# Optimization experiments

Measured on AMD Instinct MI355X. Metric: run time of the kernel, lower is better.

## Reference

```python
import jax, jax.numpy as jnp
import numpy as np

B, HIST, PRED = 16, 336, 48
S = HIST + PRED                      # 384 = max_seq_length
H, NL, NH, FF = 768, 12, 12, 3072    # default BertConfig
SA_NH = 16                           # attention_heads arg for the extra SelfAttention
V = 40000                            # num_location_ids
NE = 8                               # num_experts
D_DAY, D_TIME, D_DOW, D_WD, D_LOC = 64, 64, 64, 32, 256
D_IN = D_DAY + D_TIME + D_DOW + D_WD + D_LOC + 1  # 481


def _ln(x, g, b, eps):
    m = jnp.mean(x, -1, keepdims=True)
    v = jnp.mean(jnp.square(x - m), -1, keepdims=True)
    return (x - m) * jax.lax.rsqrt(v + eps) * g + b


def _mha(x, qW, qb, kW, kb, vW, vb, nh):
    b_, s_, h_ = x.shape
    hd = h_ // nh
    q = (x @ qW + qb).reshape(b_, s_, nh, hd)
    k = (x @ kW + kb).reshape(b_, s_, nh, hd)
    v = (x @ vW + vb).reshape(b_, s_, nh, hd)
    scores = jnp.einsum('bqhd,bkhd->bhqk', q, k) / jnp.sqrt(jnp.float32(hd))
    probs = jax.nn.softmax(scores, axis=-1)
    return jnp.einsum('bhqk,bkhd->bqhd', probs, v).reshape(b_, s_, h_)


FLOAT_NAMES = ['day_emb', 'time_emb', 'dow_emb', 'wd_emb', 'loc_emb',
               'ln_in_g', 'ln_in_b', 'inp_W', 'inp_b', 'res_W', 'res_b',
               'sa_qW', 'sa_qb', 'sa_kW', 'sa_kb', 'sa_vW', 'sa_vb', 'sa_oW', 'sa_ob', 'sa_lng', 'sa_lnb',
               'pos_emb', 'tt_emb', 'be_lng', 'be_lnb',
               'bqW', 'bqb', 'bkW', 'bkb', 'bvW', 'bvb', 'boW', 'bob', 'balng', 'balnb',
               'bf1W', 'bf1b', 'bf2W', 'bf2b', 'bflng', 'bflnb',
               'moe_W', 'moe_b', 'gate_W', 'gate_b', 'out_W', 'out_b']


def _forward(floats, ints):
    (day_emb, time_emb, dow_emb, wd_emb, loc_emb,
     ln_in_g, ln_in_b, inp_W, inp_b, res_W, res_b,
     sa_qW, sa_qb, sa_kW, sa_kb, sa_vW, sa_vb, sa_oW, sa_ob, sa_lng, sa_lnb,
     pos_emb, tt_emb, be_lng, be_lnb,
     bqW, bqb, bkW, bkb, bvW, bvb, boW, bob, balng, balnb,
     bf1W, bf1b, bf2W, bf2b, bflng, bflnb,
     moe_W, moe_b, gate_W, gate_b, out_W, out_b) = floats
    isf, hloc, psf = ints

    def feat(f):
        return (day_emb[f[:, :, 0]], time_emb[f[:, :, 1]], dow_emb[f[:, :, 3]],
                wd_emb[f[:, :, 4]], f[:, :, 5].astype(jnp.float32)[..., None])
    hd_, ht_, hw_, hwd_, hdl = feat(isf)
    hist = jnp.concatenate([hd_, ht_, hw_, hwd_, hdl, loc_emb[hloc]], -1)
    fd_, ft_, fw_, fwd_, fdl = feat(psf)
    fut_loc = jnp.zeros((psf.shape[0], psf.shape[1], D_LOC), jnp.float32)  # unknown future locations
    fut = jnp.concatenate([fd_, ft_, fw_, fwd_, fdl, fut_loc], -1)
    x = jnp.concatenate([hist, fut], 1)            # [B,S,481]
    x = _ln(x, ln_in_g, ln_in_b, 1e-5)             # layer_norm on raw features (dropout = identity in eval)
    proj = x @ inp_W + inp_b                       # input_projection -> [B,S,768]
    res = x @ res_W + res_b                        # residual_fc -> [B,S,768]

    # extra SelfAttention block (16 heads) with post-LN residual
    ctx = _mha(proj, sa_qW, sa_qb, sa_kW, sa_kb, sa_vW, sa_vb, SA_NH)
    h = _ln(ctx @ sa_oW + sa_ob + proj, sa_lng, sa_lnb, 1e-5)

    # BERT encoder (inputs_embeds path): add position + token_type(0) embeddings, then 12 post-LN layers
    h = _ln(h + pos_emb[None] + tt_emb, be_lng, be_lnb, 1e-12)
    for i in range(NL):
        ctx = _mha(h, bqW[i], bqb[i], bkW[i], bkb[i], bvW[i], bvb[i], NH)
        a = _ln(ctx @ boW[i] + bob[i] + h, balng[i], balnb[i], 1e-12)
        ff = jax.nn.gelu(a @ bf1W[i] + bf1b[i], approximate=False) @ bf2W[i] + bf2b[i]
        h = _ln(ff + a, bflng[i], bflnb[i], 1e-12)

    # dense soft-MoE: every expert runs on every token, softmax-gated sum
    xf = h.reshape(-1, H)                                                 # [B*S, H]
    eo = jax.nn.gelu(jnp.einsum('nd,edh->neh', xf, moe_W) + moe_b[None], approximate=False)
    gp = jax.nn.softmax(xf @ gate_W + gate_b, axis=-1)                     # [B*S, E]
    moe_out = jnp.einsum('ne,neh->nh', gp, eo).reshape(h.shape)

    logits = (moe_out + res) @ out_W + out_b                               # [B,S,V]
    return logits[:, HIST:, :]                                             # predictions for future slots


def setup_inputs() -> dict:
    key = jax.random.key(0)
    ctr = [0]
    def nk():
        ctr[0] += 1
        return jax.random.fold_in(key, ctr[0])
    def nrm(shape, s=0.02):
        return jax.random.normal(nk(), shape, jnp.float32) * s
    p = {}
    p['input_seq_feature'] = jax.random.randint(nk(), (B, HIST, 6), 0, 2)
    p['historical_locations'] = jax.random.randint(nk(), (B, HIST), 0, V)
    p['predict_seq_feature'] = jax.random.randint(nk(), (B, PRED, 6), 0, 2)
    p['day_emb'] = nrm((75, D_DAY)); p['time_emb'] = nrm((48, D_TIME))
    p['dow_emb'] = nrm((7, D_DOW)); p['wd_emb'] = nrm((2, D_WD)); p['loc_emb'] = nrm((V, D_LOC))
    p['ln_in_g'] = jnp.ones((D_IN,), jnp.float32); p['ln_in_b'] = jnp.zeros((D_IN,), jnp.float32)
    p['inp_W'] = nrm((D_IN, H)); p['inp_b'] = jnp.zeros((H,), jnp.float32)
    p['res_W'] = nrm((D_IN, H)); p['res_b'] = jnp.zeros((H,), jnp.float32)
    for n in ['sa_qW', 'sa_kW', 'sa_vW', 'sa_oW']:
        p[n] = nrm((H, H))
    for n in ['sa_qb', 'sa_kb', 'sa_vb', 'sa_ob']:
        p[n] = jnp.zeros((H,), jnp.float32)
    p['sa_lng'] = jnp.ones((H,), jnp.float32); p['sa_lnb'] = jnp.zeros((H,), jnp.float32)
    p['pos_emb'] = nrm((S, H)); p['tt_emb'] = nrm((H,))
    p['be_lng'] = jnp.ones((H,), jnp.float32); p['be_lnb'] = jnp.zeros((H,), jnp.float32)
    for n in ['bqW', 'bkW', 'bvW', 'boW']:
        p[n] = nrm((NL, H, H))
    for n in ['bqb', 'bkb', 'bvb', 'bob']:
        p[n] = jnp.zeros((NL, H), jnp.float32)
    p['balng'] = jnp.ones((NL, H), jnp.float32); p['balnb'] = jnp.zeros((NL, H), jnp.float32)
    p['bf1W'] = nrm((NL, H, FF)); p['bf1b'] = jnp.zeros((NL, FF), jnp.float32)
    p['bf2W'] = nrm((NL, FF, H)); p['bf2b'] = jnp.zeros((NL, H), jnp.float32)
    p['bflng'] = jnp.ones((NL, H), jnp.float32); p['bflnb'] = jnp.zeros((NL, H), jnp.float32)
    p['moe_W'] = nrm((NE, H, H)); p['moe_b'] = jnp.zeros((NE, H), jnp.float32)
    p['gate_W'] = nrm((H, NE)); p['gate_b'] = jnp.zeros((NE,), jnp.float32)
    p['out_W'] = nrm((H, V)); p['out_b'] = jnp.zeros((V,), jnp.float32)
    return p


def reference(input_seq_feature, historical_locations, predict_seq_feature,
              day_emb, time_emb, dow_emb, wd_emb, loc_emb,
              ln_in_g, ln_in_b, inp_W, inp_b, res_W, res_b,
              sa_qW, sa_qb, sa_kW, sa_kb, sa_vW, sa_vb, sa_oW, sa_ob, sa_lng, sa_lnb,
              pos_emb, tt_emb, be_lng, be_lnb,
              bqW, bqb, bkW, bkb, bvW, bvb, boW, bob, balng, balnb,
              bf1W, bf1b, bf2W, bf2b, bflng, bflnb,
              moe_W, moe_b, gate_W, gate_b, out_W, out_b):
    floats = (day_emb, time_emb, dow_emb, wd_emb, loc_emb,
              ln_in_g, ln_in_b, inp_W, inp_b, res_W, res_b,
              sa_qW, sa_qb, sa_kW, sa_kb, sa_vW, sa_vb, sa_oW, sa_ob, sa_lng, sa_lnb,
              pos_emb, tt_emb, be_lng, be_lnb,
              bqW, bqb, bkW, bkb, bvW, bvb, boW, bob, balng, balnb,
              bf1W, bf1b, bf2W, bf2b, bflng, bflnb,
              moe_W, moe_b, gate_W, gate_b, out_W, out_b)
    ints = (input_seq_feature, historical_locations, predict_seq_feature)
    return _forward(floats, ints)
```

## Files before the change

### kernel.cpp

```cpp
#include <hip/hip_runtime.h>
#include <cstddef>
#include <math.h>

#define BB 16
#define HIST 336
#define PRED 48
#define SS 384
#define HH 768
#define NL 12
#define FF_ 3072
#define DIN 481
#define DINP 512
#define NE_ 8
#define VV 40000
#define VVP 40064

typedef __attribute__((ext_vector_type(8))) short short8;
typedef __attribute__((ext_vector_type(4))) float f32x4;
struct short4v { short x, y, z, w; };

__device__ __forceinline__ short f2bf(float f) {
    union { float f; unsigned u; } v; v.f = f;
    unsigned r = v.u + 0x7fff + ((v.u >> 16) & 1);
    return (short)(r >> 16);
}
__device__ __forceinline__ float bf2f(short s) {
    union { unsigned u; float f; } v; v.u = ((unsigned)(unsigned short)s) << 16;
    return v.f;
}

using gvoid_t = const __attribute__((address_space(1))) void;
using svoid_t = __attribute__((address_space(3))) void;

template<int OP, bool SWZ>
__global__ __launch_bounds__(256)
void gemm_bf16(const short* __restrict__ A, const short* __restrict__ Bt,
               const float* __restrict__ bias, const float* __restrict__ bias2,
               const float* __restrict__ bias3,
               void* __restrict__ Cout, int Kp, int M, int ldc)
{
    __shared__ short As[2][128 * 64];
    __shared__ short Bs[2][128 * 64];
    const int tid  = threadIdx.x;
    const int lane = tid & 63;
    const int w    = tid >> 6;
    const int wr = w >> 1, wc = w & 1;
    const int lrow = lane & 15, lgrp = lane >> 4;

    int bx = blockIdx.x, by = blockIdx.y;
    if (SWZ) {
        const int nwg = gridDim.x * gridDim.y;
        const int o = blockIdx.y * gridDim.x + blockIdx.x;
        const int xcd = o & 7, k = o >> 3;
        const int q = nwg >> 3, r = nwg & 7;
        const int nid = (xcd < r ? xcd * (q + 1) : r * (q + 1) + (xcd - r) * q) + k;
        bx = nid / gridDim.y;
        by = nid % gridDim.y;
    }
    const size_t rowBase = (size_t)by * 128;
    const size_t colBase = (size_t)bx * 128;

    f32x4 acc[4][4];
    #pragma unroll
    for (int i = 0; i < 4; ++i)
        #pragma unroll
        for (int j = 0; j < 4; ++j)
            acc[i][j] = f32x4{0.f, 0.f, 0.f, 0.f};

    const int nkt = Kp >> 6;

    auto stage = [&](int buf, int kt) {
        const short* Ab = A  + rowBase * Kp + (size_t)kt * 64;
        const short* Bb = Bt + colBase * Kp + (size_t)kt * 64;
        #pragma unroll
        for (int c = 0; c < 4; ++c) {
            const int sidx = (w * 4 + c) * 64 + lane;
            const int r = sidx >> 3, sl = sidx & 7;
            const int sseg = sl ^ (r & 7);
            __builtin_amdgcn_global_load_lds(
                (gvoid_t*)(Ab + (size_t)r * Kp + sseg * 8),
                (svoid_t*)&As[buf][(w * 4 + c) * 512], 16, 0, 0);
            __builtin_amdgcn_global_load_lds(
                (gvoid_t*)(Bb + (size_t)r * Kp + sseg * 8),
                (svoid_t*)&Bs[buf][(w * 4 + c) * 512], 16, 0, 0);
        }
    };

    int cur = 0;
    stage(0, 0);
    __syncthreads();
    for (int kt = 0; kt < nkt; ++kt) {
        if (kt + 1 < nkt) stage(cur ^ 1, kt + 1);
        const short* as = As[cur];
        const short* bs = Bs[cur];
        #pragma unroll
        for (int kk = 0; kk < 2; ++kk) {
            short8 aF[4], bF[4];
            #pragma unroll
            for (int mi = 0; mi < 4; ++mi) {
                const int r = wr * 64 + mi * 16 + lrow;
                const int seg = (kk * 4 + lgrp) ^ (r & 7);
                aF[mi] = *(const short8*)&as[r * 64 + seg * 8];
            }
            #pragma unroll
            for (int ni = 0; ni < 4; ++ni) {
                const int r = wc * 64 + ni * 16 + lrow;
                const int seg = (kk * 4 + lgrp) ^ (r & 7);
                bF[ni] = *(const short8*)&bs[r * 64 + seg * 8];
            }
            #pragma unroll
            for (int mi = 0; mi < 4; ++mi)
                #pragma unroll
                for (int ni = 0; ni < 4; ++ni)
                    acc[mi][ni] = __builtin_amdgcn_mfma_f32_16x16x32_bf16(
                        aF[mi], bF[ni], acc[mi][ni], 0, 0, 0);
        }
        __syncthreads();
        cur ^= 1;
    }

    #pragma unroll
    for (int mi = 0; mi < 4; ++mi) {
        #pragma unroll
        for (int ni = 0; ni < 4; ++ni) {
            const int col = (int)colBase + wc * 64 + ni * 16 + lrow;
            if (col >= M) continue;
            const float* bp = bias; int bc = col;
            if (bias2 && col >= HH) {
                if (col < 2 * HH) { bp = bias2; bc = col - HH; }
                else              { bp = bias3; bc = col - 2 * HH; }
            }
            const float bz = bp[bc];
            #pragma unroll
            for (int j = 0; j < 4; ++j) {
                const size_t row = rowBase + wr * 64 + mi * 16 + lgrp * 4 + j;
                float v = acc[mi][ni][j] + bz;
                if (OP == 1 || OP == 4)
                    v = 0.5f * v * (1.f + erff(v * 0.70710678118654752f));
                if (OP == 4 || OP == 5) ((short*)Cout)[row * ldc + col] = f2bf(v);
                else                    ((float*)Cout)[row * ldc + col] = v;
            }
        }
    }
}

template<int HD>
__global__ __launch_bounds__(256)
void attn_mfma(const short* __restrict__ Qg, const short* __restrict__ Kg,
               const short* __restrict__ Vg, short* __restrict__ Og,
               int nh, int ldq, int ldo, float scale)
{
    constexpr int NI = HD / 16;
    constexpr int SEGS = HD / 8;
    __shared__ short Qs[64 * 64];
    __shared__ short Ks[64 * 64];
    __shared__ short Vt[64 * 72];
    __shared__ short Ps[4][16 * 80];
    int idx = blockIdx.x;
    const int qt = idx % 6; idx /= 6;
    const int h = idx % nh; idx /= nh;
    const int b = idx;
    const int tid = threadIdx.x;
    const int lane = tid & 63;
    const int w = tid >> 6;
    const int lrow = lane & 15, lgrp = lane >> 4;

    const short* Qbase = Qg + ((size_t)(b * SS + qt * 64)) * ldq + h * HD;
    #pragma unroll
    for (int t = 0; t < 2; ++t) {
        const int i = tid + t * 256;
        const int r = i >> 3, sg = i & 7;
        short8 v = {0, 0, 0, 0, 0, 0, 0, 0};
        if (sg < SEGS) v = *(const short8*)(Qbase + (size_t)r * ldq + sg * 8);
        *(short8*)&Qs[r * 64 + (sg ^ (r & 7)) * 8] = v;
    }

    float m_[4], l_[4];
    f32x4 o_[NI];
    #pragma unroll
    for (int j = 0; j < 4; ++j) { m_[j] = -1e30f; l_[j] = 0.f; }
    #pragma unroll
    for (int ni = 0; ni < NI; ++ni) o_[ni] = f32x4{0.f, 0.f, 0.f, 0.f};

    for (int kt = 0; kt < 6; ++kt) {
        const short* Kb2 = Kg + ((size_t)(b * SS + kt * 64)) * ldq + h * HD;
        const short* Vb2 = Vg + ((size_t)(b * SS + kt * 64)) * ldq + h * HD;
        __syncthreads();
        #pragma unroll
        for (int c = 0; c < 2; ++c) {
            const int r = (w * 2 + c) * 8 + (lane >> 3);
            const int sg = (lane & 7) ^ (r & 7);
            __builtin_amdgcn_global_load_lds(
                (gvoid_t*)(Kb2 + (size_t)r * ldq + sg * 8),
                (svoid_t*)&Ks[(w * 2 + c) * 512], 16, 0, 0);
        }
        for (int i = tid; i < 64 * SEGS; i += 256) {
            const int k = i & 63, sg = i >> 6;
            short8 v = *(const short8*)(Vb2 + (size_t)k * ldq + sg * 8);
            #pragma unroll
            for (int j2 = 0; j2 < 8; ++j2)
                Vt[(sg * 8 + j2) * 72 + k] = v[j2];
        }
        __syncthreads();

        f32x4 s[4];
        #pragma unroll
        for (int ni = 0; ni < 4; ++ni) s[ni] = f32x4{0.f, 0.f, 0.f, 0.f};
        __builtin_amdgcn_s_setprio(1);
        #pragma unroll
        for (int kk = 0; kk < 2; ++kk) {
            const int ra = w * 16 + lrow;
            const short8 aF = *(const short8*)&Qs[ra * 64 + ((kk * 4 + lgrp) ^ (ra & 7)) * 8];
            #pragma unroll
            for (int ni = 0; ni < 4; ++ni) {
                const int rb = ni * 16 + lrow;
                const short8 bF = *(const short8*)&Ks[rb * 64 + ((kk * 4 + lgrp) ^ (rb & 7)) * 8];
                s[ni] = __builtin_amdgcn_mfma_f32_16x16x32_bf16(aF, bF, s[ni], 0, 0, 0);
            }
        }
        __builtin_amdgcn_s_setprio(0);
        #pragma unroll
        for (int ni = 0; ni < 4; ++ni)
            #pragma unroll
            for (int j = 0; j < 4; ++j) s[ni][j] *= scale;

        #pragma unroll
        for (int j = 0; j < 4; ++j) {
            float tm = fmaxf(fmaxf(s[0][j], s[1][j]), fmaxf(s[2][j], s[3][j]));
            #pragma unroll
            for (int d = 1; d < 16; d <<= 1) tm = fmaxf(tm, __shfl_xor(tm, d));
            const float mn = fmaxf(m_[j], tm);
            const float r2 = __expf(m_[j] - mn);
            float p[4], ps = 0.f;
            #pragma unroll
            for (int ni = 0; ni < 4; ++ni) { p[ni] = __expf(s[ni][j] - mn); ps += p[ni]; }
            #pragma unroll
            for (int d = 1; d < 16; d <<= 1) ps += __shfl_xor(ps, d);
            l_[j] = l_[j] * r2 + ps;
            m_[j] = mn;
            #pragma unroll
            for (int ni = 0; ni < NI; ++ni) o_[ni][j] *= r2;
            #pragma unroll
            for (int ni = 0; ni < 4; ++ni)
                Ps[w][(lgrp * 4 + j) * 80 + ni * 16 + lrow] = f2bf(p[ni]);
        }

        __builtin_amdgcn_s_setprio(1);
        #pragma unroll
        for (int kk = 0; kk < 2; ++kk) {
            const short8 aP = *(const short8*)&Ps[w][lrow * 80 + kk * 32 + lgrp * 8];
            #pragma unroll
            for (int ni = 0; ni < NI; ++ni) {
                const int d0 = ni * 16 + lrow;
                const short8 bV = *(const short8*)&Vt[d0 * 72 + (kk * 4 + lgrp) * 8];
                o_[ni] = __builtin_amdgcn_mfma_f32_16x16x32_bf16(aP, bV, o_[ni], 0, 0, 0);
            }
        }
        __builtin_amdgcn_s_setprio(0);
    }

    const size_t orow0 = (size_t)(b * SS + qt * 64 + w * 16);
    #pragma unroll
    for (int j = 0; j < 4; ++j) {
        const float inv = 1.f / l_[j];
        #pragma unroll
        for (int ni = 0; ni < NI; ++ni)
            Og[(orow0 + lgrp * 4 + j) * ldo + h * HD + ni * 16 + lrow] =
                f2bf(o_[ni][j] * inv);
    }
}

__global__ __launch_bounds__(256)
void transpose_cvt_b(const float* __restrict__ W, short* __restrict__ Wt,
                     int K, int M, int Kp, size_t sStride, size_t dStride)
{
    __shared__ float tile[32][33];
    const float* src = W + blockIdx.z * sStride;
    short* dst = Wt + blockIdx.z * dStride;
    const int m0 = blockIdx.x * 32, k0 = blockIdx.y * 32;
    const int tx = threadIdx.x, ty = threadIdx.y;
    #pragma unroll
    for (int i = 0; i < 4; ++i) {
        int k = k0 + ty + i * 8, m = m0 + tx;
        tile[ty + i * 8][tx] = (k < K && m < M) ? src[(size_t)k * M + m] : 0.f;
    }
    __syncthreads();
    #pragma unroll
    for (int i = 0; i < 4; ++i) {
        int m = m0 + ty + i * 8, k = k0 + tx;
        dst[(size_t)m * Kp + k] = f2bf(tile[tx][ty + i * 8]);
    }
}

__global__ __launch_bounds__(256)
void prep_layer_w(const float* __restrict__ bqA, const float* __restrict__ bkA,
                  const float* __restrict__ bvA, const float* __restrict__ boA,
                  const float* __restrict__ f1A, const float* __restrict__ f2A,
                  short* __restrict__ qkvT, short* __restrict__ oT,
                  short* __restrict__ f1T, short* __restrict__ f2T)
{
    __shared__ float tile[32][33];
    const size_t L = blockIdx.y;
    const float* bq = bqA + L * HH * HH;
    const float* bk = bkA + L * HH * HH;
    const float* bv = bvA + L * HH * HH;
    const float* bo = boA + L * HH * HH;
    const float* f1 = f1A + L * HH * FF_;
    const float* f2 = f2A + L * FF_ * HH;
    short* qT = qkvT + L * 3 * HH * HH;
    short* oT2 = oT + L * HH * HH;
    short* f1T2 = f1T + L * HH * FF_;
    short* f2T2 = f2T + L * FF_ * HH;

    int id = blockIdx.x;
    const float* src; short* dst; int K, M, tm, tk;
    if (id < 1728) {
        const int mat = id / 576, r = id % 576;
        src = mat == 0 ? bq : (mat == 1 ? bk : bv);
        dst = qT + (size_t)mat * HH * HH;
        K = HH; M = HH; tm = r % 24; tk = r / 24;
    } else if (id < 2304) {
        const int r = id - 1728;
        src = bo; dst = oT2; K = HH; M = HH; tm = r % 24; tk = r / 24;
    } else if (id < 4608) {
        const int r = id - 2304;
        src = f1; dst = f1T2; K = HH; M = FF_; tm = r % 96; tk = r / 96;
    } else {
        const int r = id - 4608;
        src = f2; dst = f2T2; K = FF_; M = HH; tm = r % 24; tk = r / 24;
    }
    const int m0 = tm * 32, k0 = tk * 32;
    const int tx = threadIdx.x & 31, ty = threadIdx.x >> 5;
    #pragma unroll
    for (int i = 0; i < 4; ++i) {
        int k = k0 + ty + i * 8, m = m0 + tx;
        tile[ty + i * 8][tx] = src[(size_t)k * M + m];
    }
    __syncthreads();
    #pragma unroll
    for (int i = 0; i < 4; ++i) {
        int m = m0 + ty + i * 8, k = k0 + tx;
        dst[(size_t)m * K + k] = f2bf(tile[tx][ty + i * 8]);
    }
}

__global__ __launch_bounds__(256)
void cvt_bf16(const float* __restrict__ src, short* __restrict__ dst, int n4)
{
    int i = blockIdx.x * 256 + threadIdx.x;
    if (i >= n4) return;
    float4 v = reinterpret_cast<const float4*>(src)[i];
    short4v o = { f2bf(v.x), f2bf(v.y), f2bf(v.z), f2bf(v.w) };
    reinterpret_cast<short4v*>(dst)[i] = o;
}

__global__ __launch_bounds__(512)
void build_x(const int* __restrict__ isf, const int* __restrict__ hloc,
             const int* __restrict__ psf,
             const float* __restrict__ dayE, const float* __restrict__ timeE,
             const float* __restrict__ dowE, const float* __restrict__ wdE,
             const float* __restrict__ locE,
             const float* __restrict__ g, const float* __restrict__ b2,
             short* __restrict__ xb)
{
    const int tok = blockIdx.x;
    const int b = tok / SS, s = tok % SS;
    const int tid = threadIdx.x;
    __shared__ float red[512];
    const int* f;
    int loc = -1;
    if (s < HIST) { f = isf + (b * HIST + s) * 6; loc = hloc[b * HIST + s]; }
    else          { f = psf + (b * PRED + (s - HIST)) * 6; }
    float val = 0.f;
    if (tid < DIN) {
        int c = tid;
        if      (c < 64)  val = dayE[f[0] * 64 + c];
        else if (c < 128) val = timeE[f[1] * 64 + (c - 64)];
        else if (c < 192) val = dowE[f[3] * 64 + (c - 128)];
        else if (c < 224) val = wdE[f[4] * 32 + (c - 192)];
        else if (c == 224) val = (float)f[5];
        else val = (loc >= 0) ? locE[(size_t)loc * 256 + (c - 225)] : 0.f;
    }
    red[tid] = (tid < DIN) ? val : 0.f;
    __syncthreads();
    for (int o = 256; o > 0; o >>= 1) { if (tid < o) red[tid] += red[tid + o]; __syncthreads(); }
    float mean = red[0] / (float)DIN;
    __syncthreads();
    float d = (tid < DIN) ? (val - mean) : 0.f;
    red[tid] = d * d;
    __syncthreads();
    for (int o = 256; o > 0; o >>= 1) { if (tid < o) red[tid] += red[tid + o]; __syncthreads(); }
    float rstd = rsqrtf(red[0] / (float)DIN + 1e-5f);
    if (tid < DINP)
        xb[(size_t)tok * DINP + tid] =
            (tid < DIN) ? f2bf((val - mean) * rstd * g[tid] + b2[tid]) : (short)0;
}

__global__ __launch_bounds__(256)
void ln768b(short* __restrict__ out, const short* __restrict__ in1,
            const short* __restrict__ in2,
            const float* __restrict__ g, const float* __restrict__ b2,
            float eps)
{
    const int w = threadIdx.x >> 6, lane = threadIdx.x & 63;
    const int row = blockIdx.x * 4 + w;
    float t[12];
    float sum = 0.f;
    #pragma unroll
    for (int i = 0; i < 3; ++i) {
        const int c = i * 256 + lane * 4;
        short4v a = *(const short4v*)&in1[(size_t)row * HH + c];
        short4v b = *(const short4v*)&in2[(size_t)row * HH + c];
        t[i * 4 + 0] = bf2f(a.x) + bf2f(b.x);
        t[i * 4 + 1] = bf2f(a.y) + bf2f(b.y);
        t[i * 4 + 2] = bf2f(a.z) + bf2f(b.z);
        t[i * 4 + 3] = bf2f(a.w) + bf2f(b.w);
        sum += t[i*4] + t[i*4+1] + t[i*4+2] + t[i*4+3];
    }
    #pragma unroll
    for (int d = 1; d < 64; d <<= 1) sum += __shfl_xor(sum, d);
    const float mean = sum * (1.f / 768.f);
    float p2 = 0.f;
    #pragma unroll
    for (int i = 0; i < 12; ++i) { float d = t[i] - mean; p2 += d * d; }
    #pragma unroll
    for (int d = 1; d < 64; d <<= 1) p2 += __shfl_xor(p2, d);
    const float rstd = rsqrtf(p2 * (1.f / 768.f) + eps);
    #pragma unroll
    for (int i = 0; i < 3; ++i) {
        const int c = i * 256 + lane * 4;
        float4 gg = *(const float4*)&g[c];
        float4 bb = *(const float4*)&b2[c];
        short4v ob = { f2bf((t[i*4+0] - mean) * rstd * gg.x + bb.x),
                       f2bf((t[i*4+1] - mean) * rstd * gg.y + bb.y),
                       f2bf((t[i*4+2] - mean) * rstd * gg.z + bb.z),
                       f2bf((t[i*4+3] - mean) * rstd * gg.w + bb.w) };
        *(short4v*)&out[(size_t)row * HH + c] = ob;
    }
}

__global__ __launch_bounds__(256)
void ln2_fused(short* __restrict__ out, const short* __restrict__ in1,
               const short* __restrict__ in2,
               const float* __restrict__ pos, const float* __restrict__ tt,
               const float* __restrict__ g1, const float* __restrict__ b1,
               const float* __restrict__ g2, const float* __restrict__ b2)
{
    const int w = threadIdx.x >> 6, lane = threadIdx.x & 63;
    const int row = blockIdx.x * 4 + w;
    const int s = row % SS;
    float t[12];
    float sum = 0.f;
    #pragma unroll
    for (int i = 0; i < 3; ++i) {
        const int c = i * 256 + lane * 4;
        short4v a = *(const short4v*)&in1[(size_t)row * HH + c];
        short4v b = *(const short4v*)&in2[(size_t)row * HH + c];
        t[i*4+0] = bf2f(a.x) + bf2f(b.x);
        t[i*4+1] = bf2f(a.y) + bf2f(b.y);
        t[i*4+2] = bf2f(a.z) + bf2f(b.z);
        t[i*4+3] = bf2f(a.w) + bf2f(b.w);
        sum += t[i*4] + t[i*4+1] + t[i*4+2] + t[i*4+3];
    }
    #pragma unroll
    for (int d = 1; d < 64; d <<= 1) sum += __shfl_xor(sum, d);
    float mean = sum * (1.f / 768.f);
    float p2 = 0.f;
    #pragma unroll
    for (int i = 0; i < 12; ++i) { float d = t[i] - mean; p2 += d * d; }
    #pragma unroll
    for (int d = 1; d < 64; d <<= 1) p2 += __shfl_xor(p2, d);
    float rstd = rsqrtf(p2 * (1.f / 768.f) + 1e-5f);
    sum = 0.f;
    #pragma unroll
    for (int i = 0; i < 3; ++i) {
        const int c = i * 256 + lane * 4;
        float4 gg = *(const float4*)&g1[c];
        float4 bb = *(const float4*)&b1[c];
        float4 pp = *(const float4*)&pos[(size_t)s * HH + c];
        float4 tz = *(const float4*)&tt[c];
        t[i*4+0] = (t[i*4+0] - mean) * rstd * gg.x + bb.x + pp.x + tz.x;
        t[i*4+1] = (t[i*4+1] - mean) * rstd * gg.y + bb.y + pp.y + tz.y;
        t[i*4+2] = (t[i*4+2] - mean) * rstd * gg.z + bb.z + pp.z + tz.z;
        t[i*4+3] = (t[i*4+3] - mean) * rstd * gg.w + bb.w + pp.w + tz.w;
        sum += t[i*4] + t[i*4+1] + t[i*4+2] + t[i*4+3];
    }
    #pragma unroll
    for (int d = 1; d < 64; d <<= 1) sum += __shfl_xor(sum, d);
    mean = sum * (1.f / 768.f);
    p2 = 0.f;
    #pragma unroll
    for (int i = 0; i < 12; ++i) { float d = t[i] - mean; p2 += d * d; }
    #pragma unroll
    for (int d = 1; d < 64; d <<= 1) p2 += __shfl_xor(p2, d);
    rstd = rsqrtf(p2 * (1.f / 768.f) + 1e-12f);
    #pragma unroll
    for (int i = 0; i < 3; ++i) {
        const int c = i * 256 + lane * 4;
        float4 gg = *(const float4*)&g2[c];
        float4 bb = *(const float4*)&b2[c];
        short4v ob = { f2bf((t[i*4+0] - mean) * rstd * gg.x + bb.x),
                       f2bf((t[i*4+1] - mean) * rstd * gg.y + bb.y),
                       f2bf((t[i*4+2] - mean) * rstd * gg.z + bb.z),
                       f2bf((t[i*4+3] - mean) * rstd * gg.w + bb.w) };
        *(short4v*)&out[(size_t)row * HH + c] = ob;
    }
}

__global__ void gather_fut_b16(const short* __restrict__ src, short* __restrict__ dst, int D)
{
    const int r = blockIdx.x;
    const int b = r / PRED, t = r % PRED;
    const int srow = b * SS + HIST + t;
    for (int c = threadIdx.x; c < D; c += blockDim.x)
        dst[(size_t)r * D + c] = src[(size_t)srow * D + c];
}

__global__ __launch_bounds__(256)
void gate_kernel(const short* __restrict__ Xb, const float* __restrict__ Wg,
                 const float* __restrict__ bg, float* __restrict__ out)
{
    const int row = blockIdx.x;
    const int tid = threadIdx.x;
    float a[NE_] = {};
    for (int k = tid; k < HH; k += 256) {
        float xv = bf2f(Xb[(size_t)row * HH + k]);
        #pragma unroll
        for (int e = 0; e < NE_; ++e) a[e] = fmaf(xv, Wg[k * NE_ + e], a[e]);
    }
    __shared__ float red[256];
    #pragma unroll
    for (int e = 0; e < NE_; ++e) {
        red[tid] = a[e]; __syncthreads();
        for (int o = 128; o > 0; o >>= 1) { if (tid < o) red[tid] += red[tid + o]; __syncthreads(); }
        if (tid == 0) out[(size_t)row * NE_ + e] = red[0] + bg[e];
        __syncthreads();
    }
}

__global__ void gate_softmax(float* __restrict__ gate)
{
    const int r = blockIdx.x * blockDim.x + threadIdx.x;
    if (r >= BB * PRED) return;
    float* p = gate + (size_t)r * NE_;
    float mx = p[0];
    for (int e = 1; e < NE_; ++e) mx = fmaxf(mx, p[e]);
    float s = 0.f, v[NE_];
    for (int e = 0; e < NE_; ++e) { v[e] = __expf(p[e] - mx); s += v[e]; }
    for (int e = 0; e < NE_; ++e) p[e] = v[e] / s;
}

__global__ __launch_bounds__(256)
void moe_reduce(const float* __restrict__ eo, const float* __restrict__ gp,
                float* __restrict__ futm)
{
    const int row = blockIdx.x;
    float g[NE_];
    #pragma unroll
    for (int e = 0; e < NE_; ++e) g[e] = gp[row * NE_ + e];
    for (int c = threadIdx.x; c < HH; c += 256) {
        float s = futm[(size_t)row * HH + c];
        #pragma unroll
        for (int e = 0; e < NE_; ++e)
            s = fmaf(g[e], eo[(size_t)row * (NE_ * HH) + e * HH + c], s);
        futm[(size_t)row * HH + c] = s;
    }
}

extern "C" void kernel_launch(void* const* d_in, const int* in_sizes, int n_in,
                              void* d_out, int out_size, void* d_ws, size_t ws_size,
                              hipStream_t stream)
{
    const int*   isf   = (const int*)  d_in[0];
    const int*   hloc  = (const int*)  d_in[1];
    const int*   psf   = (const int*)  d_in[2];
    const float* dayE  = (const float*)d_in[3];
    const float* timeE = (const float*)d_in[4];
    const float* dowE  = (const float*)d_in[5];
    const float* wdE   = (const float*)d_in[6];
    const float* locE  = (const float*)d_in[7];
    const float* ln_g  = (const float*)d_in[8];
    const float* ln_b  = (const float*)d_in[9];
    const float* inpW  = (const float*)d_in[10];
    const float* inpB  = (const float*)d_in[11];
    const float* resW  = (const float*)d_in[12];
    const float* resB  = (const float*)d_in[13];
    const float* saqW  = (const float*)d_in[14];
    const float* sakW  = (const float*)d_in[15];
    const float* savW  = (const float*)d_in[16];
    const float* saoW  = (const float*)d_in[17];
    const float* saqB  = (const float*)d_in[18];
    const float* sakB  = (const float*)d_in[19];
    const float* savB  = (const float*)d_in[20];
    const float* saoB  = (const float*)d_in[21];
    const float* salnG = (const float*)d_in[22];
    const float* salnB = (const float*)d_in[23];
    const float* posE  = (const float*)d_in[24];
    const float* ttE   = (const float*)d_in[25];
    const float* belnG = (const float*)d_in[26];
    const float* belnB = (const float*)d_in[27];
    const float* bqW   = (const float*)d_in[28];
    const float* bkW   = (const float*)d_in[29];
    const float* bvW   = (const float*)d_in[30];
    const float* boW   = (const float*)d_in[31];
    const float* bqB   = (const float*)d_in[32];
    const float* bkB   = (const float*)d_in[33];
    const float* bvB   = (const float*)d_in[34];
    const float* boB   = (const float*)d_in[35];
    const float* balnG = (const float*)d_in[36];
    const float* balnB = (const float*)d_in[37];
    const float* bf1W  = (const float*)d_in[38];
    const float* bf1B  = (const float*)d_in[39];
    const float* bf2W  = (const float*)d_in[40];
    const float* bf2B  = (const float*)d_in[41];
    const float* bflnG = (const float*)d_in[42];
    const float* bflnB = (const float*)d_in[43];
    const float* moeW  = (const float*)d_in[44];
    const float* moeB  = (const float*)d_in[45];
    const float* gateW = (const float*)d_in[46];
    const float* gateB = (const float*)d_in[47];
    const float* outW  = (const float*)d_in[48];
    const float* outB  = (const float*)d_in[49];

    const int N6 = BB * SS;
    const int NF = BB * PRED;

    char* base = (char*)d_ws;
    size_t off = 0;
    auto alloc = [&](size_t bytes) -> void* {
        void* p = base + off;
        off = (off + bytes + 255) & ~(size_t)255;
        return p;
    };

    short* xb   = (short*)alloc((size_t)N6 * DINP * 2);
    short* pb   = (short*)alloc((size_t)N6 * HH * 2);
    short* ab   = (short*)alloc((size_t)N6 * HH * 2);
    short* Ob   = (short*)alloc((size_t)N6 * HH * 2);
    short* hcur = (short*)alloc((size_t)N6 * HH * 2);
    short* QKVb = (short*)alloc((size_t)N6 * 3 * HH * 2);
    short* C16  = (short*)alloc((size_t)N6 * HH * 2);
    short* ffb  = (short*)alloc((size_t)N6 * FF_ * 2);
    short* inpWt  = (short*)alloc((size_t)HH * DINP * 2);
    short* resWt  = (short*)alloc((size_t)HH * DINP * 2);
    short* saWt   = (short*)alloc((size_t)3 * HH * HH * 2);
    short* saoWt  = (short*)alloc((size_t)HH * HH * 2);
    short* lqkvWt = (short*)alloc((size_t)3 * HH * HH * 2);
    short* loWt   = (short*)alloc((size_t)HH * HH * 2);
    short* lf1Wt  = (short*)alloc((size_t)FF_ * HH * 2);
    short* lf2Wt  = (short*)alloc((size_t)HH * FF_ * 2);
    float* futm   = (float*)alloc((size_t)NF * HH * 4);
    float* futg   = (float*)alloc((size_t)NF * NE_ * 4);

    const size_t perL = ((size_t)3*HH*HH + (size_t)HH*HH + (size_t)HH*FF_ + (size_t)FF_*HH) * 2;
    short* LqkvA = nullptr; short* LoA = nullptr; short* Lf1A = nullptr; short* Lf2A = nullptr;
    bool upfront = false;
    if (ws_size > off + 12 * perL + (32u << 20)) {
        LqkvA = (short*)alloc((size_t)12 * 3 * HH * HH * 2);
        LoA   = (short*)alloc((size_t)12 * HH * HH * 2);
        Lf1A  = (short*)alloc((size_t)12 * HH * FF_ * 2);
        Lf2A  = (short*)alloc((size_t)12 * FF_ * HH * 2);
        upfront = true;
    }

    short* outWt = QKVb;
    short* moeWt = outWt + (size_t)VVP * HH;
    short* futhb = moeWt + (size_t)NE_ * HH * HH;
    short* futxb = futhb + (size_t)NF * HH;
    short* futmb = futxb + (size_t)NF * DINP;
    float* eoF   = (float*)pb;

    build_x<<<N6, 512, 0, stream>>>(isf, hloc, psf, dayE, timeE, dowE, wdE, locE,
                                    ln_g, ln_b, xb);

    dim3 tb(32, 8);
    transpose_cvt_b<<<dim3(HH/32, DINP/32, 1), tb, 0, stream>>>(inpW, inpWt, DIN, HH, DINP, 0, 0);
    transpose_cvt_b<<<dim3(HH/32, DINP/32, 1), tb, 0, stream>>>(resW, resWt, DIN, HH, DINP, 0, 0);
    transpose_cvt_b<<<dim3(HH/32, HH/32, 1), tb, 0, stream>>>(saqW, saWt,                   HH, HH, HH, 0, 0);
    transpose_cvt_b<<<dim3(HH/32, HH/32, 1), tb, 0, stream>>>(sakW, saWt + (size_t)HH*HH,   HH, HH, HH, 0, 0);
    transpose_cvt_b<<<dim3(HH/32, HH/32, 1), tb, 0, stream>>>(savW, saWt + (size_t)2*HH*HH, HH, HH, HH, 0, 0);
    transpose_cvt_b<<<dim3(HH/32, HH/32, 1), tb, 0, stream>>>(saoW, saoWt, HH, HH, HH, 0, 0);
    if (upfront)
        prep_layer_w<<<dim3(6912, 12), 256, 0, stream>>>(
            bqW, bkW, bvW, boW, bf1W, bf2W, LqkvA, LoA, Lf1A, Lf2A);

    gemm_bf16<5, false><<<dim3(HH/128, N6/128), 256, 0, stream>>>(
        xb, inpWt, inpB, nullptr, nullptr, pb, DINP, HH, HH);

    gemm_bf16<5, false><<<dim3(3*HH/128, N6/128), 256, 0, stream>>>(
        pb, saWt, saqB, sakB, savB, QKVb, HH, 3*HH, 3*HH);
    attn_mfma<48><<<BB*16*6, 256, 0, stream>>>(
        QKVb, QKVb + HH, QKVb + 2*HH, Ob, 16, 3*HH, HH, 1.f / sqrtf(48.f));
    gemm_bf16<5, false><<<dim3(HH/128, N6/128), 256, 0, stream>>>(
        Ob, saoWt, saoB, nullptr, nullptr, C16, HH, HH, HH);
    ln2_fused<<<N6/4, 256, 0, stream>>>(hcur, C16, pb, posE, ttE,
                                        salnG, salnB, belnG, belnB);

    for (int i = 0; i < NL; ++i) {
        const size_t bo = (size_t)i * HH;
        const short* wQ; const short* wO; const short* wF1; const short* wF2;
        if (upfront) {
            wQ  = LqkvA + (size_t)i * 3 * HH * HH;
            wO  = LoA   + (size_t)i * HH * HH;
            wF1 = Lf1A  + (size_t)i * HH * FF_;
            wF2 = Lf2A  + (size_t)i * FF_ * HH;
        } else {
            prep_layer_w<<<dim3(6912, 1), 256, 0, stream>>>(
                bqW + (size_t)i*HH*HH, bkW + (size_t)i*HH*HH, bvW + (size_t)i*HH*HH,
                boW + (size_t)i*HH*HH, bf1W + (size_t)i*HH*FF_, bf2W + (size_t)i*FF_*HH,
                lqkvWt, loWt, lf1Wt, lf2Wt);
            wQ = lqkvWt; wO = loWt; wF1 = lf1Wt; wF2 = lf2Wt;
        }

        gemm_bf16<5, false><<<dim3(3*HH/128, N6/128), 256, 0, stream>>>(
            hcur, wQ, bqB + bo, bkB + bo, bvB + bo, QKVb, HH, 3*HH, 3*HH);
        attn_mfma<64><<<BB*12*6, 256, 0, stream>>>(
            QKVb, QKVb + HH, QKVb + 2*HH, Ob, 12, 3*HH, HH, 0.125f);
        gemm_bf16<5, false><<<dim3(HH/128, N6/128), 256, 0, stream>>>(
            Ob, wO, boB + bo, nullptr, nullptr, C16, HH, HH, HH);
        ln768b<<<N6/4, 256, 0, stream>>>(ab, C16, hcur, balnG + bo, balnB + bo, 1e-12f);
        gemm_bf16<4, false><<<dim3(FF_/128, N6/128), 256, 0, stream>>>(
            ab, wF1, bf1B + (size_t)i * FF_, nullptr, nullptr, ffb, HH, FF_, FF_);
        gemm_bf16<5, false><<<dim3(HH/128, N6/128), 256, 0, stream>>>(
            ffb, wF2, bf2B + bo, nullptr, nullptr, C16, FF_, HH, HH);
        ln768b<<<N6/4, 256, 0, stream>>>(hcur, C16, ab, bflnG + bo, bflnB + bo, 1e-12f);
    }

    gather_fut_b16<<<NF, 256, 0, stream>>>(hcur, futhb, HH);
    gather_fut_b16<<<NF, 256, 0, stream>>>(xb, futxb, DINP);

    gemm_bf16<0, false><<<dim3(HH/128, NF/128), 256, 0, stream>>>(
        futxb, resWt, resB, nullptr, nullptr, futm, DINP, HH, HH);

    gate_kernel<<<NF, 256, 0, stream>>>(futhb, gateW, gateB, futg);
    gate_softmax<<<3, 256, 0, stream>>>(futg);

    transpose_cvt_b<<<dim3(HH/32, HH/32, NE_), tb, 0, stream>>>(
        moeW, moeWt, HH, HH, HH, (size_t)HH*HH, (size_t)HH*HH);
    gemm_bf16<1, true><<<dim3(NE_*HH/128, NF/128), 256, 0, stream>>>(
        futhb, moeWt, moeB, nullptr, nullptr, eoF, HH, NE_*HH, NE_*HH);
    moe_reduce<<<NF, 256, 0, stream>>>(eoF, futg, futm);

    {
        int n4 = (int)((size_t)NF * HH / 4);
        cvt_bf16<<<(n4 + 255) / 256, 256, 0, stream>>>(futm, futmb, n4);
    }
    transpose_cvt_b<<<dim3(VVP/32, HH/32, 1), tb, 0, stream>>>(
        outW, outWt, HH, VV, HH, 0, 0);
    gemm_bf16<0, true><<<dim3(VVP/128, NF/128), 256, 0, stream>>>(
        futmb, outWt, outB, nullptr, nullptr, (float*)d_out, HH, VV, VV);
}
```

Measured before the change: 3.663 ms.

## Add 256x256-tile double-buffered bf16 GEMM for QKV and FFN1 projections

Adds a new GEMM kernel with 256x256 output tiles, 512 threads, and double-buffered LDS staging through global_load_lds with XOR swizzle. It is used for the wide QKV and FF1 projections in place of the 128x128 kernel. Larger tiles raise arithmetic intensity and cut global reloads of A and B. The cost is 128KB of LDS per block, so only one block fits per CU, and far fewer blocks are launched. With N6=6144 rows, QKV gets 9x24=216 blocks and FF1 gets 12x24=288, which may leave some of the 256 CUs underused.

Result: slower. 4.597 ms (+25.5%).

```diff
diff --git a/kernel.cpp b/kernel.cpp
--- a/kernel.cpp
+++ b/kernel.cpp
@@ -139,6 +139,105 @@
                     v = 0.5f * v * (1.f + erff(v * 0.70710678118654752f));
                 if (OP == 4 || OP == 5) ((short*)Cout)[row * ldc + col] = f2bf(v);
                 else                    ((float*)Cout)[row * ldc + col] = v;
+            }
+        }
+    }
+}
+
+template<int OP>
+__global__ __launch_bounds__(512, 1)
+void gemm256_bf16(const short* __restrict__ A, const short* __restrict__ Bt,
+                  const float* __restrict__ bias, const float* __restrict__ bias2,
+                  const float* __restrict__ bias3,
+                  void* __restrict__ Cout, int Kp, int M, int ldc)
+{
+    __shared__ short As[2][256 * 64];
+    __shared__ short Bs[2][256 * 64];
+    const int tid  = threadIdx.x;
+    const int lane = tid & 63;
+    const int w    = tid >> 6;
+    const int wr = w >> 2, wc = w & 3;
+    const int lrow = lane & 15, lgrp = lane >> 4;
+    const size_t rowBase = (size_t)blockIdx.y * 256;
+    const size_t colBase = (size_t)blockIdx.x * 256;
+
+    f32x4 acc[8][4];
+    #pragma unroll
+    for (int i = 0; i < 8; ++i)
+        #pragma unroll
+        for (int j = 0; j < 4; ++j)
+            acc[i][j] = f32x4{0.f, 0.f, 0.f, 0.f};
+
+    const int nkt = Kp >> 6;
+
+    auto stage = [&](int buf, int kt) {
+        const short* Ab = A  + rowBase * Kp + (size_t)kt * 64;
+        const short* Bb = Bt + colBase * Kp + (size_t)kt * 64;
+        #pragma unroll
+        for (int c = 0; c < 4; ++c) {
+            const int sidx = c * 512 + w * 64 + lane;
+            const int r = sidx >> 3, sl = sidx & 7;
+            const int sseg = sl ^ (r & 7);
+            __builtin_amdgcn_global_load_lds(
+                (gvoid_t*)(Ab + (size_t)r * Kp + sseg * 8),
+                (svoid_t*)&As[buf][(c * 512 + w * 64) * 8], 16, 0, 0);
+            __builtin_amdgcn_global_load_lds(
+                (gvoid_t*)(Bb + (size_t)r * Kp + sseg * 8),
+                (svoid_t*)&Bs[buf][(c * 512 + w * 64) * 8], 16, 0, 0);
+        }
+    };
+
+    int cur = 0;
+    stage(0, 0);
+    __syncthreads();
+    for (int kt = 0; kt < nkt; ++kt) {
+        if (kt + 1 < nkt) stage(cur ^ 1, kt + 1);
+        const short* as = As[cur];
+        const short* bs = Bs[cur];
+        #pragma unroll
+        for (int kk = 0; kk < 2; ++kk) {
+            short8 aF[8], bF[4];
+            #pragma unroll
+            for (int mi = 0; mi < 8; ++mi) {
+                const int r = wr * 128 + mi * 16 + lrow;
+                const int seg = (kk * 4 + lgrp) ^ (r & 7);
+                aF[mi] = *(const short8*)&as[r * 64 + seg * 8];
+            }
+            #pragma unroll
+            for (int ni = 0; ni < 4; ++ni) {
+                const int r = wc * 64 + ni * 16 + lrow;
+                const int seg = (kk * 4 + lgrp) ^ (r & 7);
+                bF[ni] = *(const short8*)&bs[r * 64 + seg * 8];
+            }
+            #pragma unroll
+            for (int mi = 0; mi < 8; ++mi)
+                #pragma unroll
+                for (int ni = 0; ni < 4; ++ni)
+                    acc[mi][ni] = __builtin_amdgcn_mfma_f32_16x16x32_bf16(
+                        aF[mi], bF[ni], acc[mi][ni], 0, 0, 0);
+        }
+        __syncthreads();
+        cur ^= 1;
+    }
+
+    #pragma unroll
+    for (int mi = 0; mi < 8; ++mi) {
+        #pragma unroll
+        for (int ni = 0; ni < 4; ++ni) {
+            const int col = (int)colBase + wc * 64 + ni * 16 + lrow;
+            if (col >= M) continue;
+            const float* bp = bias; int bc = col;
+            if (bias2 && col >= HH) {
+                if (col < 2 * HH) { bp = bias2; bc = col - HH; }
+                else              { bp = bias3; bc = col - 2 * HH; }
+            }
+            const float bz = bp[bc];
+            #pragma unroll
+            for (int j = 0; j < 4; ++j) {
+                const size_t row = rowBase + wr * 128 + mi * 16 + lgrp * 4 + j;
+                float v = acc[mi][ni][j] + bz;
+                if (OP == 4) v = 0.5f * v * (1.f + erff(v * 0.70710678118654752f));
+                ((short*)Cout)[row * ldc + col] = f2bf(v);
             }
         }
     }
@@ -687,7 +786,7 @@
     gemm_bf16<5, false><<<dim3(HH/128, N6/128), 256, 0, stream>>>(
         xb, inpWt, inpB, nullptr, nullptr, pb, DINP, HH, HH);
 
-    gemm_bf16<5, false><<<dim3(3*HH/128, N6/128), 256, 0, stream>>>(
+    gemm256_bf16<5><<<dim3(3*HH/256, N6/256), 512, 0, stream>>>(
         pb, saWt, saqB, sakB, savB, QKVb, HH, 3*HH, 3*HH);
     attn_mfma<48><<<BB*16*6, 256, 0, stream>>>(
         QKVb, QKVb + HH, QKVb + 2*HH, Ob, 16, 3*HH, HH, 1.f / sqrtf(48.f));
@@ -712,14 +811,14 @@
             wQ = lqkvWt; wO = loWt; wF1 = lf1Wt; wF2 = lf2Wt;
         }
 
-        gemm_bf16<5, false><<<dim3(3*HH/128, N6/128), 256, 0, stream>>>(
+        gemm256_bf16<5><<<dim3(3*HH/256, N6/256), 512, 0, stream>>>(
             hcur, wQ, bqB + bo, bkB + bo, bvB + bo, QKVb, HH, 3*HH, 3*HH);
         attn_mfma<64><<<BB*12*6, 256, 0, stream>>>(
             QKVb, QKVb + HH, QKVb + 2*HH, Ob, 12, 3*HH, HH, 0.125f);
         gemm_bf16<5, false><<<dim3(HH/128, N6/128), 256, 0, stream>>>(
             Ob, wO, boB + bo, nullptr, nullptr, C16, HH, HH, HH);
         ln768b<<<N6/4, 256, 0, stream>>>(ab, C16, hcur, balnG + bo, balnB + bo, 1e-12f);
-        gemm_bf16<4, false><<<dim3(FF_/128, N6/128), 256, 0, stream>>>(
+        gemm256_bf16<4><<<dim3(FF_/256, N6/256), 512, 0, stream>>>(
             ab, wF1, bf1B + (size_t)i * FF_, nullptr, nullptr, ffb, HH, FF_, FF_);
         gemm_bf16<5, false><<<dim3(HH/128, N6/128), 256, 0, stream>>>(
             ffb, wF2, bf2B + bo, nullptr, nullptr, C16, FF_, HH, HH);
```

## Compute only future-token rows in final BERT layer after QKV projection

Applied to the files above, without the earlier changes.

In the last encoder layer, attention is run only for the final 64-query tile of each sequence, since only the last 48 positions feed the output head. The attention output and residual rows for those tiles are gathered into compact buffers, and the output projection, layernorms and FFN run on 1024 rows instead of 6144. This removes about five sixths of the last layer's post-QKV work, in exchange for extra gather kernels and buffers. The final future-row gather is remapped to read from the compact buffer.

Result: no change. 3.593 ms (-1.9%).

```diff
diff --git a/kernel.cpp b/kernel.cpp
--- a/kernel.cpp
+++ b/kernel.cpp
@@ -14,6 +14,7 @@
 #define NE_ 8
 #define VV 40000
 #define VVP 40064
+#define NT 1024
 
 typedef __attribute__((ext_vector_type(8))) short short8;
 typedef __attribute__((ext_vector_type(4))) float f32x4;
@@ -148,7 +149,7 @@
 __global__ __launch_bounds__(256)
 void attn_mfma(const short* __restrict__ Qg, const short* __restrict__ Kg,
                const short* __restrict__ Vg, short* __restrict__ Og,
-               int nh, int ldq, int ldo, float scale)
+               int nh, int ldq, int ldo, float scale, int qt0, int nqt)
 {
     constexpr int NI = HD / 16;
     constexpr int SEGS = HD / 8;
@@ -157,7 +158,7 @@
     __shared__ short Vt[64 * 72];
     __shared__ short Ps[4][16 * 80];
     int idx = blockIdx.x;
-    const int qt = idx % 6; idx /= 6;
+    const int qt = qt0 + idx % nqt; idx /= nqt;
     const int h = idx % nh; idx /= nh;
     const int b = idx;
     const int tid = threadIdx.x;
@@ -507,11 +508,12 @@
     }
 }
 
-__global__ void gather_fut_b16(const short* __restrict__ src, short* __restrict__ dst, int D)
+__global__ void gather_rows_b16(const short* __restrict__ src, short* __restrict__ dst,
+                                int D, int srcGroup, int srcOff, int dstGroup)
 {
     const int r = blockIdx.x;
-    const int b = r / PRED, t = r % PRED;
-    const int srow = b * SS + HIST + t;
+    const int b = r / dstGroup, t = r % dstGroup;
+    const int srow = b * srcGroup + srcOff + t;
     for (int c = threadIdx.x; c < D; c += blockDim.x)
         dst[(size_t)r * D + c] = src[(size_t)srow * D + c];
 }
@@ -651,6 +653,12 @@
     short* lf2Wt  = (short*)alloc((size_t)HH * FF_ * 2);
     float* futm   = (float*)alloc((size_t)NF * HH * 4);
     float* futg   = (float*)alloc((size_t)NF * NE_ * 4);
+    short* Og   = (short*)alloc((size_t)NT * HH * 2);
+    short* hg   = (short*)alloc((size_t)NT * HH * 2);
+    short* Cg   = (short*)alloc((size_t)NT * HH * 2);
+    short* ag   = (short*)alloc((size_t)NT * HH * 2);
+    short* hfg  = (short*)alloc((size_t)NT * HH * 2);
+    short* ffg  = (short*)alloc((size_t)NT * FF_ * 2);
 
     const size_t perL = ((size_t)3*HH*HH + (size_t)HH*HH + (size_t)HH*FF_ + (size_t)FF_*HH) * 2;
     short* LqkvA = nullptr; short* LoA = nullptr; short* Lf1A = nullptr; short* Lf2A = nullptr;
@@ -690,7 +698,7 @@
     gemm_bf16<5, false><<<dim3(3*HH/128, N6/128), 256, 0, stream>>>(
         pb, saWt, saqB, sakB, savB, QKVb, HH, 3*HH, 3*HH);
     attn_mfma<48><<<BB*16*6, 256, 0, stream>>>(
-        QKVb, QKVb + HH, QKVb + 2*HH, Ob, 16, 3*HH, HH, 1.f / sqrtf(48.f));
+        QKVb, QKVb + HH, QKVb + 2*HH, Ob, 16, 3*HH, HH, 1.f / sqrtf(48.f), 0, 6);
     gemm_bf16<5, false><<<dim3(HH/128, N6/128), 256, 0, stream>>>(
         Ob, saoWt, saoB, nullptr, nullptr, C16, HH, HH, HH);
     ln2_fused<<<N6/4, 256, 0, stream>>>(hcur, C16, pb, posE, ttE,
@@ -714,20 +722,36 @@
 
         gemm_bf16<5, false><<<dim3(3*HH/128, N6/128), 256, 0, stream>>>(
             hcur, wQ, bqB + bo, bkB + bo, bvB + bo, QKVb, HH, 3*HH, 3*HH);
-        attn_mfma<64><<<BB*12*6, 256, 0, stream>>>(
-            QKVb, QKVb + HH, QKVb + 2*HH, Ob, 12, 3*HH, HH, 0.125f);
-        gemm_bf16<5, false><<<dim3(HH/128, N6/128), 256, 0, stream>>>(
-            Ob, wO, boB + bo, nullptr, nullptr, C16, HH, HH, HH);
-        ln768b<<<N6/4, 256, 0, stream>>>(ab, C16, hcur, balnG + bo, balnB + bo, 1e-12f);
-        gemm_bf16<4, false><<<dim3(FF_/128, N6/128), 256, 0, stream>>>(
-            ab, wF1, bf1B + (size_t)i * FF_, nullptr, nullptr, ffb, HH, FF_, FF_);
-        gemm_bf16<5, false><<<dim3(HH/128, N6/128), 256, 0, stream>>>(
-            ffb, wF2, bf2B + bo, nullptr, nullptr, C16, FF_, HH, HH);
-        ln768b<<<N6/4, 256, 0, stream>>>(hcur, C16, ab, bflnG + bo, bflnB + bo, 1e-12f);
-    }
-
-    gather_fut_b16<<<NF, 256, 0, stream>>>(hcur, futhb, HH);
-    gather_fut_b16<<<NF, 256, 0, stream>>>(xb, futxb, DINP);
+
+        if (i < NL - 1) {
+            attn_mfma<64><<<BB*12*6, 256, 0, stream>>>(
+                QKVb, QKVb + HH, QKVb + 2*HH, Ob, 12, 3*HH, HH, 0.125f, 0, 6);
+            gemm_bf16<5, false><<<dim3(HH/128, N6/128), 256, 0, stream>>>(
+                Ob, wO, boB + bo, nullptr, nullptr, C16, HH, HH, HH);
+            ln768b<<<N6/4, 256, 0, stream>>>(ab, C16, hcur, balnG + bo, balnB + bo, 1e-12f);
+            gemm_bf16<4, false><<<dim3(FF_/128, N6/128), 256, 0, stream>>>(
+                ab, wF1, bf1B + (size_t)i * FF_, nullptr, nullptr, ffb, HH, FF_, FF_);
+            gemm_bf16<5, false><<<dim3(HH/128, N6/128), 256, 0, stream>>>(
+                ffb, wF2, bf2B + bo, nullptr, nullptr, C16, FF_, HH, HH);
+            ln768b<<<N6/4, 256, 0, stream>>>(hcur, C16, ab, bflnG + bo, bflnB + bo, 1e-12f);
+        } else {
+            attn_mfma<64><<<BB*12*1, 256, 0, stream>>>(
+                QKVb, QKVb + HH, QKVb + 2*HH, Ob, 12, 3*HH, HH, 0.125f, 5, 1);
+            gather_rows_b16<<<NT, 256, 0, stream>>>(Ob,   Og, HH, SS, 320, 64);
+            gather_rows_b16<<<NT, 256, 0, stream>>>(hcur, hg, HH, SS, 320, 64);
+            gemm_bf16<5, false><<<dim3(HH/128, NT/128), 256, 0, stream>>>(
+                Og, wO, boB + bo, nullptr, nullptr, Cg, HH, HH, HH);
+            ln768b<<<NT/4, 256, 0, stream>>>(ag, Cg, hg, balnG + bo, balnB + bo, 1e-12f);
+            gemm_bf16<4, false><<<dim3(FF_/128, NT/128), 256, 0, stream>>>(
+                ag, wF1, bf1B + (size_t)i * FF_, nullptr, nullptr, ffg, HH, FF_, FF_);
+            gemm_bf16<5, false><<<dim3(HH/128, NT/128), 256, 0, stream>>>(
+                ffg, wF2, bf2B + bo, nullptr, nullptr, Cg, FF_, HH, HH);
+            ln768b<<<NT/4, 256, 0, stream>>>(hfg, Cg, ag, bflnG + bo, bflnB + bo, 1e-12f);
+        }
+    }
+
+    gather_rows_b16<<<NF, 256, 0, stream>>>(hfg, futhb, HH, 64, 16, PRED);
+    gather_rows_b16<<<NF, 256, 0, stream>>>(xb, futxb, DINP, SS, HIST, PRED);
 
     gemm_bf16<0, false><<<dim3(HH/128, NF/128), 256, 0, stream>>>(
         futxb, resWt, resB, nullptr, nullptr, futm, DINP, HH, HH);
```
